# Kernel optimization log

Measured on AMD Instinct MI355X. Metric: run time of the kernel, lower is better.

## Reference

```python
import jax, jax.numpy as jnp
import numpy as np

B, NQ, NK, DM, H, DK = 8, 1024, 1024, 512, 8, 64


def setup_inputs() -> dict:
    key = jax.random.key(0)
    ks = jax.random.split(key, 20)
    s = 1.0 / np.sqrt(DM)
    inp = {
        "queries": jax.random.normal(ks[0], (B, NQ, DM), jnp.float32),
        "keys": jax.random.normal(ks[1], (B, NK, DM), jnp.float32),
        "values": jax.random.normal(ks[2], (B, NK, DM), jnp.float32),
        "attention_mask": jax.random.randint(ks[3], (B, H, NQ, NK), 0, 2).astype(bool),
        "attention_weights": jax.random.uniform(ks[4], (B, H, NQ, NK), jnp.float32),
        "memory": jax.random.uniform(ks[5], (B, NK), jnp.float32),
        "geometry": jax.random.uniform(ks[6], (B, H, NQ, NK), jnp.float32),
        "Wq": jax.random.normal(ks[7], (DM, H * DK), jnp.float32) * s,
        "bq": jnp.zeros((H * DK,), jnp.float32),
        "Wk": jax.random.normal(ks[8], (DM, H * DK), jnp.float32) * s,
        "bk": jnp.zeros((H * DK,), jnp.float32),
        "Wv": jax.random.normal(ks[9], (DM, H * DK), jnp.float32) * s,
        "bv": jnp.zeros((H * DK,), jnp.float32),
        "Wmm": jax.random.normal(ks[10], (1, H * DK), jnp.float32),
        "bmm": jnp.zeros((H * DK,), jnp.float32),
        "Wo": jax.random.normal(ks[11], (H * DK, DM), jnp.float32) * s,
        "bo": jnp.zeros((DM,), jnp.float32),
    }
    return inp


def reference(queries, keys, values, attention_mask, attention_weights, memory,
              geometry, Wq, bq, Wk, bk, Wv, bv, Wmm, bmm, Wo, bo):
    b, nq = queries.shape[:2]
    nk = keys.shape[1]
    # projections -> (b, h, n, d)
    q = (queries @ Wq + bq).reshape(b, nq, H, DK).transpose(0, 2, 1, 3)
    k = (keys @ Wk + bk).reshape(b, nk, H, DK).transpose(0, 2, 1, 3)
    v = (values @ Wv + bv).reshape(b, nk, H, DK).transpose(0, 2, 1, 3)
    # memory gate: (b, nk, 1) @ (1, h*dk) -> (b, h, nk, dk)
    mm = (memory[..., None] @ Wmm + bmm).reshape(b, nk, H, DK).transpose(0, 2, 1, 3)
    # gated scores (b, h, nq, nk)
    att = jnp.einsum('bhqd,bhkd->bhqk', q, k * mm) / np.sqrt(DK)
    att = att * attention_weights
    att = jnp.where(attention_mask, -jnp.inf, att)
    # geometric log-bias + softmax
    w_mn = jax.nn.softmax(jnp.log(jnp.clip(geometry, 1e-6)) + att, axis=-1)
    out = jnp.einsum('bhqk,bhkd->bhqd', w_mn, v * mm)
    out = out.transpose(0, 2, 1, 3).reshape(b, nq, H * DK)
    return out @ Wo + bo
```

## Files before the change

kernel.cpp:

```cpp
#include <hip/hip_runtime.h>
#include <hip/hip_bf16.h>
#include <math.h>

#define B_ 8
#define NQ_ 1024
#define NK_ 1024
#define H_ 8
#define DK_ 64
#define HDK_ 512
#define LOG2E 1.4426950408889634f

typedef _Float16 half8 __attribute__((ext_vector_type(8)));
typedef _Float16 half4 __attribute__((ext_vector_type(4)));
typedef float f32x4 __attribute__((ext_vector_type(4)));

__global__ __launch_bounds__(256)
void wtrans_kernel(const float* __restrict__ w0, const float* __restrict__ w1,
                   const float* __restrict__ w2, const float* __restrict__ w3,
                   _Float16* __restrict__ t0, _Float16* __restrict__ t1,
                   _Float16* __restrict__ t2, _Float16* __restrict__ t3,
                   const unsigned int* __restrict__ maskw, int nwords,
                   int* __restrict__ flag) {
  __shared__ float tile[64][65];
  if (blockIdx.x == 64) {
    if (blockIdx.y != 0) return;
    __shared__ int s;
    if (threadIdx.x == 0) s = 0;
    __syncthreads();
    int bad = 0;
    for (int i = threadIdx.x; i < nwords; i += blockDim.x) {
      unsigned int v = maskw[i];
      if (v > 1u && v != 0x3F800000u) bad = 1;
    }
    if (bad) atomicOr(&s, 1);
    __syncthreads();
    if (threadIdx.x == 0) *flag = s;
    return;
  }
  const float* W;
  _Float16* T;
  switch (blockIdx.y) {
    case 0: W = w0; T = t0; break;
    case 1: W = w1; T = t1; break;
    case 2: W = w2; T = t2; break;
    default: W = w3; T = t3; break;
  }
  const int t = blockIdx.x;
  const int k0 = (t >> 3) * 64, n0 = (t & 7) * 64;
  const int tid = threadIdx.x;
  const int r = tid >> 4, c4 = (tid & 15) * 4;
#pragma unroll
  for (int i = 0; i < 4; ++i) {
    const int kk = r + i * 16;
    float4 v = *(const float4*)(W + (size_t)(k0 + kk) * 512 + n0 + c4);
    tile[kk][c4 + 0] = v.x;
    tile[kk][c4 + 1] = v.y;
    tile[kk][c4 + 2] = v.z;
    tile[kk][c4 + 3] = v.w;
  }
  __syncthreads();
#pragma unroll
  for (int i = 0; i < 4; ++i) {
    const int nn = r + i * 16;
    half4 h;
#pragma unroll
    for (int j = 0; j < 4; ++j) h[j] = (_Float16)tile[c4 + j][nn];
    *(half4*)(T + (size_t)(n0 + nn) * 512 + k0 + c4) = h;
  }
}

__global__ __launch_bounds__(256)
void gemm_kernel(const float* __restrict__ A0, const float* __restrict__ A1,
                 const float* __restrict__ A2, const _Float16* __restrict__ A16,
                 const _Float16* __restrict__ B0, const _Float16* __restrict__ B1,
                 const _Float16* __restrict__ B2, const float* __restrict__ bias0,
                 const float* __restrict__ bias1, const float* __restrict__ bias2,
                 const float* __restrict__ mem, const float* __restrict__ Wmm,
                 const float* __restrict__ bmm, void* __restrict__ out0,
                 void* __restrict__ out1, void* __restrict__ out2,
                 const int mode_base) {
  __shared__ _Float16 As[128 * 32];
  __shared__ _Float16 Bs[128 * 32];
  const int mode = mode_base + blockIdx.z;
  const float* A32 = (mode == 1) ? A1 : (mode == 2) ? A2 : A0;
  const _Float16* Bt = (mode == 1) ? B1 : (mode == 2) ? B2 : B0;
  const float* bias = (mode == 1) ? bias1 : (mode == 2) ? bias2 : bias0;
  void* outp = (mode == 1) ? out1 : (mode == 2) ? out2 : out0;

  const int tid = threadIdx.x;
  const int lane = tid & 63, wave = tid >> 6;
  const int wr = wave >> 1, wc = wave & 1;
  const int l15 = lane & 15, l4 = lane >> 4;
  const int row0 = blockIdx.x * 128, col0 = blockIdx.y * 128;
  const int srow = tid >> 1;
  const int sc0 = (tid & 1) * 2;

  f32x4 acc[4][4] = {};

  for (int k0 = 0; k0 < 512; k0 += 32) {
    __syncthreads();
    const _Float16* sb = Bt + (size_t)(col0 + srow) * 512 + k0;
#pragma unroll
    for (int c = 0; c < 2; ++c) {
      int ci = sc0 + c;
      half8 ha;
      if (mode == 3) {
        ha = *(const half8*)(A16 + (size_t)(row0 + srow) * 512 + k0 + ci * 8);
      } else {
        const float* s = A32 + (size_t)(row0 + srow) * 512 + k0 + ci * 8;
        float4 x = *(const float4*)s;
        float4 y = *(const float4*)(s + 4);
        ha[0] = (_Float16)x.x; ha[1] = (_Float16)x.y;
        ha[2] = (_Float16)x.z; ha[3] = (_Float16)x.w;
        ha[4] = (_Float16)y.x; ha[5] = (_Float16)y.y;
        ha[6] = (_Float16)y.z; ha[7] = (_Float16)y.w;
      }
      float4 vb = *(const float4*)(sb + ci * 8);
      int cd = ci ^ (srow & 3);
      *(half8*)((char*)As + srow * 64 + (cd << 4)) = ha;
      *(float4*)((char*)Bs + srow * 64 + (cd << 4)) = vb;
    }
    __syncthreads();
    half8 af[4], bf[4];
#pragma unroll
    for (int mi = 0; mi < 4; ++mi) {
      int r = wr * 64 + mi * 16 + l15;
      af[mi] = *(half8*)((char*)As + r * 64 + ((l4 ^ (r & 3)) << 4));
    }
#pragma unroll
    for (int ni = 0; ni < 4; ++ni) {
      int r = wc * 64 + ni * 16 + l15;
      bf[ni] = *(half8*)((char*)Bs + r * 64 + ((l4 ^ (r & 3)) << 4));
    }
#pragma unroll
    for (int mi = 0; mi < 4; ++mi)
#pragma unroll
      for (int ni = 0; ni < 4; ++ni)
        acc[mi][ni] =
            __builtin_amdgcn_mfma_f32_16x16x32_f16(af[mi], bf[ni], acc[mi][ni], 0, 0, 0);
  }

#pragma unroll
  for (int mi = 0; mi < 4; ++mi) {
#pragma unroll
    for (int ni = 0; ni < 4; ++ni) {
      const int gc = col0 + wc * 64 + ni * 16 + l15;
      const float bi = bias[gc];
      const int h = gc >> 6, d = gc & 63;
#pragma unroll
      for (int reg = 0; reg < 4; ++reg) {
        const int gr = row0 + wr * 64 + mi * 16 + l4 * 4 + reg;
        float val = acc[mi][ni][reg] + bi;
        if (mode == 3) {
          ((float*)outp)[(size_t)gr * 512 + gc] = val;
        } else if (mode == 0) {
          const int b = gr >> 10, n = gr & 1023;
          ((_Float16*)outp)[((size_t)(b * 8 + h) * 1024 + n) * 64 + d] =
              (_Float16)(val * (LOG2E / 8.0f));
        } else {
          const int b = gr >> 10, n = gr & 1023;
          float mmv = fmaf(mem[gr], Wmm[gc], bmm[gc]);
          float g = val * mmv;
          if (mode == 1)
            ((_Float16*)outp)[((size_t)(b * 8 + h) * 1024 + n) * 64 + d] = (_Float16)g;
          else
            ((_Float16*)outp)[((size_t)(b * 8 + h) * 64 + d) * 1024 + n] = (_Float16)g;
        }
      }
    }
  }
}

__global__ __launch_bounds__(256, 4)
void attn_kernel(const _Float16* __restrict__ Qp, const _Float16* __restrict__ Kg,
                 const _Float16* __restrict__ Vgt, const float* __restrict__ attw,
                 const float* __restrict__ geom, const void* __restrict__ maskp,
                 const int* __restrict__ flagp, _Float16* __restrict__ Ocat) {
  __shared__ _Float16 Kw[4][32 * 64];
  __shared__ _Float16 Vw[4][64 * 32];
  __shared__ _Float16 Ps[4][16 * 32];

  const int tid = threadIdx.x;
  const int lane = tid & 63, wave = tid >> 6;
  const int l15 = lane & 15, l4 = lane >> 4;
  const int bid = blockIdx.x;
  const int qt = bid >> 6;
  const int g = bid & 63;
  const int h = g & 7, b = g >> 3;
  const int bh = b * H_ + h;
  const int qb = qt * 64 + wave * 16;
  const int kq = qb + l15;
  const int maskBytes = *flagp;
  const unsigned char* m8 = (const unsigned char*)maskp;
  const int* m32 = (const int*)maskp;

  half8 aq[2];
  {
    const _Float16* qsrc = Qp + ((size_t)bh * NQ_ + kq) * DK_;
#pragma unroll
    for (int s = 0; s < 2; ++s) aq[s] = *(const half8*)(qsrc + s * 32 + l4 * 8);
  }

  f32x4 fo[4] = {};
  float mrun = -INFINITY, lrun = 0.f;

  const _Float16* Kbase = Kg + (size_t)bh * NK_ * DK_;
  const _Float16* Vbase = Vgt + (size_t)bh * DK_ * NK_;
  const size_t wgBase = ((size_t)bh << 20) + (size_t)kq * NK_ + l4 * 4;

  char* const KwB = (char*)&Kw[wave][0];
  char* const VwB = (char*)&Vw[wave][0];

  auto stageK = [&](int kt) {
    const char* kgb = (const char*)(Kbase + (size_t)(kt * 32) * DK_);
#pragma unroll
    for (int i = 0; i < 4; ++i) {
      const int r = i * 8 + (lane >> 3);
      const int chunk = lane & 7;
      const char* src = kgb + (size_t)r * 128 + ((chunk ^ (r & 7)) << 4);
      __builtin_amdgcn_global_load_lds(src, KwB + i * 1024, 16, 0, 0);
    }
  };
  auto stageV = [&](int kt) {
    const char* vgb = (const char*)(Vbase + kt * 32);
#pragma unroll
    for (int i = 0; i < 4; ++i) {
      const int r = i * 16 + (lane >> 2);
      const char* src = vgb + (size_t)r * (NK_ * 2) + ((lane & 3) << 4);
      __builtin_amdgcn_global_load_lds(src, VwB + i * 1024, 16, 0, 0);
    }
  };

  float4 wv[2], gv[2];
  unsigned mk;
  auto loadWG = [&](int kt) {
    const size_t base = wgBase + (size_t)kt * 32;
    unsigned m = 0;
#pragma unroll
    for (int c = 0; c < 2; ++c) {
      wv[c] = *(const float4*)(attw + base + c * 16);
      gv[c] = *(const float4*)(geom + base + c * 16);
    }
    if (maskBytes) {
      unsigned v0 = *(const unsigned*)(m8 + base);
      unsigned v1 = *(const unsigned*)(m8 + base + 16);
      m = (((v0 & 0xffu) ? 1u : 0u) | ((v0 & 0xff00u) ? 2u : 0u) |
           ((v0 & 0xff0000u) ? 4u : 0u) | ((v0 & 0xff000000u) ? 8u : 0u)) |
          ((((v1 & 0xffu) ? 1u : 0u) | ((v1 & 0xff00u) ? 2u : 0u) |
            ((v1 & 0xff0000u) ? 4u : 0u) | ((v1 & 0xff000000u) ? 8u : 0u)) << 4);
    } else {
      int4 v0 = *(const int4*)(m32 + base);
      int4 v1 = *(const int4*)(m32 + base + 16);
      m = ((v0.x ? 1u : 0u) | (v0.y ? 2u : 0u) | (v0.z ? 4u : 0u) | (v0.w ? 8u : 0u)) |
          (((v1.x ? 1u : 0u) | (v1.y ? 2u : 0u) | (v1.z ? 4u : 0u) | (v1.w ? 8u : 0u))
           << 4);
    }
    mk = m;
  };

  stageK(0);
  loadWG(0);
  stageV(0);

  for (int kt = 0; kt < 32; ++kt) {
    f32x4 sf[2];
    __builtin_amdgcn_s_setprio(1);
#pragma unroll
    for (int c = 0; c < 2; ++c) {
      sf[c] = (f32x4){0.f, 0.f, 0.f, 0.f};
#pragma unroll
      for (int s = 0; s < 2; ++s) {
        int r = c * 16 + l15;
        half8 ak = *(half8*)(KwB + r * 128 + (((s * 4 + l4) ^ (r & 7)) << 4));
        sf[c] = __builtin_amdgcn_mfma_f32_16x16x32_f16(ak, aq[s], sf[c], 0, 0, 0);
      }
    }
    __builtin_amdgcn_s_setprio(0);

    if (kt + 1 < 32) {
      asm volatile("s_waitcnt lgkmcnt(0)" ::: "memory");
      stageK(kt + 1);
      __builtin_amdgcn_sched_barrier(0);
    }

    float mx = -INFINITY;
#pragma unroll
    for (int c = 0; c < 2; ++c)
#pragma unroll
      for (int reg = 0; reg < 4; ++reg) {
        float sv = sf[c][reg] * wv[c][reg];
        sf[c][reg] = sv;
        mx = fmaxf(mx, sv);
      }
    mx = fmaxf(mx, __shfl_xor(mx, 16));
    mx = fmaxf(mx, __shfl_xor(mx, 32));
    const float mn = fmaxf(mrun, mx);
    const float sc = (mrun == -INFINITY) ? 0.f : exp2f(mrun - mn);
    mrun = mn;

    float rs = 0.f;
#pragma unroll
    for (int c = 0; c < 2; ++c)
#pragma unroll
      for (int reg = 0; reg < 4; ++reg) {
        float p = fmaxf(gv[c][reg], 1e-6f) * exp2f(sf[c][reg] - mn);
        p = ((mk >> (c * 4 + reg)) & 1u) ? 0.f : p;
        sf[c][reg] = p;
        rs += p;
      }

    if (kt + 1 < 32) {
      loadWG(kt + 1);
      __builtin_amdgcn_sched_barrier(0);
    }

#pragma unroll
    for (int c = 0; c < 4; ++c)
#pragma unroll
      for (int reg = 0; reg < 4; ++reg) fo[c][reg] *= sc;
    lrun = lrun * sc + rs;

    char* pw = (char*)&Ps[wave][0];
#pragma unroll
    for (int c = 0; c < 2; ++c) {
      half4 hp;
#pragma unroll
      for (int reg = 0; reg < 4; ++reg) hp[reg] = (_Float16)sf[c][reg];
      *(half4*)(pw + l15 * 64 + c * 32 + l4 * 8) = hp;
    }

    half8 pa = *(half8*)(pw + l15 * 64 + l4 * 16);
    __builtin_amdgcn_s_setprio(1);
#pragma unroll
    for (int c = 0; c < 4; ++c) {
      half8 bv = *(half8*)(VwB + (c * 16 + l15) * 64 + l4 * 16);
      fo[c] = __builtin_amdgcn_mfma_f32_16x16x32_f16(bv, pa, fo[c], 0, 0, 0);
    }
    __builtin_amdgcn_s_setprio(0);

    if (kt + 1 < 32) {
      asm volatile("s_waitcnt lgkmcnt(0)" ::: "memory");
      stageV(kt + 1);
    }
  }

  float lsum = lrun;
  lsum += __shfl_xor(lsum, 16);
  lsum += __shfl_xor(lsum, 32);
  const float rinv = 1.0f / lsum;

  _Float16* orow = Ocat + ((size_t)b * NQ_ + kq) * HDK_ + h * DK_;
#pragma unroll
  for (int c = 0; c < 4; ++c) {
    half4 hv;
#pragma unroll
    for (int reg = 0; reg < 4; ++reg) hv[reg] = (_Float16)(fo[c][reg] * rinv);
    *(half4*)(orow + c * 16 + l4 * 4) = hv;
  }
}

extern "C" void kernel_launch(void* const* d_in, const int* in_sizes, int n_in,
                              void* d_out, int out_size, void* d_ws, size_t ws_size,
                              hipStream_t stream) {
  (void)in_sizes; (void)n_in; (void)out_size; (void)ws_size;
  const float* queries = (const float*)d_in[0];
  const float* keys    = (const float*)d_in[1];
  const float* values  = (const float*)d_in[2];
  const void*  maskp   = d_in[3];
  const float* attw    = (const float*)d_in[4];
  const float* memo    = (const float*)d_in[5];
  const float* geom    = (const float*)d_in[6];
  const float* Wq = (const float*)d_in[7];
  const float* bq = (const float*)d_in[8];
  const float* Wk = (const float*)d_in[9];
  const float* bk = (const float*)d_in[10];
  const float* Wv = (const float*)d_in[11];
  const float* bv = (const float*)d_in[12];
  const float* Wmm = (const float*)d_in[13];
  const float* bmm = (const float*)d_in[14];
  const float* Wo = (const float*)d_in[15];
  const float* bo = (const float*)d_in[16];

  char* ws = (char*)d_ws;
  size_t off = 0;
  auto alloc = [&](size_t bytes) {
    char* p = ws + off;
    off += (bytes + 255) & ~(size_t)255;
    return p;
  };
  const size_t MAT = (size_t)8192 * 512 * 2;
  int* flag = (int*)alloc(256);
  _Float16* Wtq = (_Float16*)alloc((size_t)512 * 512 * 2);
  _Float16* Wtk = (_Float16*)alloc((size_t)512 * 512 * 2);
  _Float16* Wtv = (_Float16*)alloc((size_t)512 * 512 * 2);
  _Float16* Wto = (_Float16*)alloc((size_t)512 * 512 * 2);
  _Float16* Qp   = (_Float16*)alloc(MAT);
  _Float16* Kgp  = (_Float16*)alloc(MAT);
  _Float16* Vgtp = (_Float16*)alloc(MAT);
  _Float16* Ocat = (_Float16*)alloc(MAT);

  wtrans_kernel<<<dim3(65, 4), 256, 0, stream>>>(Wq, Wk, Wv, Wo, Wtq, Wtk, Wtv, Wto,
                                                 (const unsigned int*)maskp, 4096, flag);

  gemm_kernel<<<dim3(64, 4, 3), 256, 0, stream>>>(
      queries, keys, values, nullptr, Wtq, Wtk, Wtv, bq, bk, bv, memo, Wmm, bmm,
      Qp, Kgp, Vgtp, 0);

  attn_kernel<<<1024, 256, 0, stream>>>(Qp, Kgp, Vgtp, attw, geom, maskp, flag, Ocat);

  gemm_kernel<<<dim3(64, 4, 1), 256, 0, stream>>>(
      nullptr, nullptr, nullptr, Ocat, Wto, nullptr, nullptr, bo, nullptr, nullptr,
      nullptr, nullptr, nullptr, d_out, nullptr, nullptr, 3);
}
```

Before: 325.5 us.

## Stage K/V through registers and double-buffer weight/geometry loads two tiles ahead

Replaces the direct global-to-LDS async loads for K and V with register prefetch of the next tile, written to LDS after the current tile's compute. Attention weights, geometry and mask are now loaded two iterations ahead into alternating register sets, with the loop unrolled by two. V and P LDS rows are padded to 80 bytes to avoid bank conflicts. Occupancy hint drops from 4 to 2 blocks per CU to fit the extra registers, which gives up some latency hiding from other waves.

Measured after the change: 325.0 us. Within noise of the previous version (-0.2%).

```diff
diff --git a/kernel.cpp b/kernel.cpp
--- a/kernel.cpp
+++ b/kernel.cpp
@@ -171,14 +171,14 @@
   }
 }
 
-__global__ __launch_bounds__(256, 4)
+__global__ __launch_bounds__(256, 2)
 void attn_kernel(const _Float16* __restrict__ Qp, const _Float16* __restrict__ Kg,
                  const _Float16* __restrict__ Vgt, const float* __restrict__ attw,
                  const float* __restrict__ geom, const void* __restrict__ maskp,
                  const int* __restrict__ flagp, _Float16* __restrict__ Ocat) {
-  __shared__ _Float16 Kw[4][32 * 64];
-  __shared__ _Float16 Vw[4][64 * 32];
-  __shared__ _Float16 Ps[4][16 * 32];
+  __shared__ char Kw[4][32 * 128];
+  __shared__ char Vw[4][64 * 80];
+  __shared__ char Pw[4][16 * 80];
 
   const int tid = threadIdx.x;
   const int lane = tid & 63, wave = tid >> 6;
@@ -208,39 +208,52 @@
   const _Float16* Vbase = Vgt + (size_t)bh * DK_ * NK_;
   const size_t wgBase = ((size_t)bh << 20) + (size_t)kq * NK_ + l4 * 4;
 
-  char* const KwB = (char*)&Kw[wave][0];
-  char* const VwB = (char*)&Vw[wave][0];
-
-  auto stageK = [&](int kt) {
-    const char* kgb = (const char*)(Kbase + (size_t)(kt * 32) * DK_);
+  char* const KwB = &Kw[wave][0];
+  char* const VwB = &Vw[wave][0];
+  char* const PwB = &Pw[wave][0];
+
+  half8 kreg[4], vreg[4];
+  const int krow = lane >> 3, kchk = lane & 7;
+  const int vrow = lane >> 2, vchk = lane & 3;
+  auto loadKreg = [&](int kt) {
+    const _Float16* kp = Kbase + (size_t)(kt * 32) * DK_;
+#pragma unroll
+    for (int i = 0; i < 4; ++i)
+      kreg[i] = *(const half8*)(kp + (size_t)(i * 8 + krow) * DK_ + kchk * 8);
+  };
+  auto writeK = [&]() {
 #pragma unroll
     for (int i = 0; i < 4; ++i) {
-      const int r = i * 8 + (lane >> 3);
-      const int chunk = lane & 7;
-      const char* src = kgb + (size_t)r * 128 + ((chunk ^ (r & 7)) << 4);
-      __builtin_amdgcn_global_load_lds(src, KwB + i * 1024, 16, 0, 0);
-    }
-  };
-  auto stageV = [&](int kt) {
-    const char* vgb = (const char*)(Vbase + kt * 32);
+      const int r = i * 8 + krow;
+      *(half8*)(KwB + r * 128 + ((kchk ^ (r & 7)) << 4)) = kreg[i];
+    }
+  };
+  auto loadVreg = [&](int kt) {
+    const _Float16* vp = Vbase + kt * 32;
+#pragma unroll
+    for (int i = 0; i < 4; ++i)
+      vreg[i] = *(const half8*)(vp + (size_t)(i * 16 + vrow) * NK_ + vchk * 8);
+  };
+  auto writeV = [&]() {
 #pragma unroll
     for (int i = 0; i < 4; ++i) {
-      const int r = i * 16 + (lane >> 2);
-      const char* src = vgb + (size_t)r * (NK_ * 2) + ((lane & 3) << 4);
-      __builtin_amdgcn_global_load_lds(src, VwB + i * 1024, 16, 0, 0);
-    }
-  };
-
-  float4 wv[2], gv[2];
-  unsigned mk;
-  auto loadWG = [&](int kt) {
+      const int r = i * 16 + vrow;
+      *(half8*)(VwB + r * 80 + vchk * 16) = vreg[i];
+    }
+  };
+
+  float4 wvA[2], gvA[2];
+  unsigned mkA;
+  float4 wvB[2], gvB[2];
+  unsigned mkB;
+  auto loadWG = [&](int kt, float4 (&wv)[2], float4 (&gv)[2], unsigned& mk) {
     const size_t base = wgBase + (size_t)kt * 32;
-    unsigned m = 0;
 #pragma unroll
     for (int c = 0; c < 2; ++c) {
       wv[c] = *(const float4*)(attw + base + c * 16);
       gv[c] = *(const float4*)(geom + base + c * 16);
     }
+    unsigned m;
     if (maskBytes) {
       unsigned v0 = *(const unsigned*)(m8 + base);
       unsigned v1 = *(const unsigned*)(m8 + base + 16);
@@ -258,11 +271,12 @@
     mk = m;
   };
 
-  stageK(0);
-  loadWG(0);
-  stageV(0);
-
-  for (int kt = 0; kt < 32; ++kt) {
+  auto ITER = [&](int t, float4 (&wvC)[2], float4 (&gvC)[2], unsigned& mkC) {
+    if (t + 1 < 32) {
+      loadKreg(t + 1);
+      loadVreg(t + 1);
+    }
+
     f32x4 sf[2];
     __builtin_amdgcn_s_setprio(1);
 #pragma unroll
@@ -277,18 +291,12 @@
     }
     __builtin_amdgcn_s_setprio(0);
 
-    if (kt + 1 < 32) {
-      asm volatile("s_waitcnt lgkmcnt(0)" ::: "memory");
-      stageK(kt + 1);
-      __builtin_amdgcn_sched_barrier(0);
-    }
-
     float mx = -INFINITY;
 #pragma unroll
     for (int c = 0; c < 2; ++c)
 #pragma unroll
       for (int reg = 0; reg < 4; ++reg) {
-        float sv = sf[c][reg] * wv[c][reg];
+        float sv = sf[c][reg] * wvC[c][reg];
         sf[c][reg] = sv;
         mx = fmaxf(mx, sv);
       }
@@ -303,16 +311,13 @@
     for (int c = 0; c < 2; ++c)
 #pragma unroll
       for (int reg = 0; reg < 4; ++reg) {
-        float p = fmaxf(gv[c][reg], 1e-6f) * exp2f(sf[c][reg] - mn);
-        p = ((mk >> (c * 4 + reg)) & 1u) ? 0.f : p;
+        float p = fmaxf(gvC[c][reg], 1e-6f) * exp2f(sf[c][reg] - mn);
+        p = ((mkC >> (c * 4 + reg)) & 1u) ? 0.f : p;
         sf[c][reg] = p;
         rs += p;
       }
 
-    if (kt + 1 < 32) {
-      loadWG(kt + 1);
-      __builtin_amdgcn_sched_barrier(0);
-    }
+    if (t + 2 < 32) loadWG(t + 2, wvC, gvC, mkC);
 
 #pragma unroll
     for (int c = 0; c < 4; ++c)
@@ -320,28 +325,38 @@
       for (int reg = 0; reg < 4; ++reg) fo[c][reg] *= sc;
     lrun = lrun * sc + rs;
 
-    char* pw = (char*)&Ps[wave][0];
+    if (t + 1 < 32) writeK();
+
 #pragma unroll
     for (int c = 0; c < 2; ++c) {
       half4 hp;
 #pragma unroll
       for (int reg = 0; reg < 4; ++reg) hp[reg] = (_Float16)sf[c][reg];
-      *(half4*)(pw + l15 * 64 + c * 32 + l4 * 8) = hp;
-    }
-
-    half8 pa = *(half8*)(pw + l15 * 64 + l4 * 16);
+      *(half4*)(PwB + l15 * 80 + c * 32 + l4 * 8) = hp;
+    }
+
+    half8 pa = *(half8*)(PwB + l15 * 80 + l4 * 16);
     __builtin_amdgcn_s_setprio(1);
 #pragma unroll
     for (int c = 0; c < 4; ++c) {
-      half8 bv = *(half8*)(VwB + (c * 16 + l15) * 64 + l4 * 16);
+      half8 bv = *(half8*)(VwB + (c * 16 + l15) * 80 + l4 * 16);
       fo[c] = __builtin_amdgcn_mfma_f32_16x16x32_f16(bv, pa, fo[c], 0, 0, 0);
     }
     __builtin_amdgcn_s_setprio(0);
 
-    if (kt + 1 < 32) {
-      asm volatile("s_waitcnt lgkmcnt(0)" ::: "memory");
-      stageV(kt + 1);
-    }
+    if (t + 1 < 32) writeV();
+  };
+
+  loadKreg(0);
+  loadVreg(0);
+  loadWG(0, wvA, gvA, mkA);
+  loadWG(1, wvB, gvB, mkB);
+  writeK();
+  writeV();
+
+  for (int kt = 0; kt < 32; kt += 2) {
+    ITER(kt, wvA, gvA, mkA);
+    ITER(kt + 1, wvB, gvB, mkB);
   }
 
   float lsum = lrun;
```
